# Kernel optimization log

Measured on AMD Instinct MI355X. Metric: run time of the kernel, lower is better.

Reference implementation:

```python
import jax, jax.numpy as jnp
import numpy as np

N_SRC = 50000
N_DST = 10000
E = 1600000
H = 1
F = 128
NEG_SLOPE = 0.2  # GAT default leaky_relu slope


def setup_inputs() -> dict:
    key = jax.random.key(0)
    k1, k2, k3, k4, k5, k6 = jax.random.split(key, 6)
    x_src = jax.random.normal(k1, (N_SRC, H, F), dtype=jnp.float32)
    x_dst = jax.random.normal(k2, (N_DST, H, F), dtype=jnp.float32)
    attn_l = jax.random.normal(k3, (1, H, F), dtype=jnp.float32)
    attn_r = jax.random.normal(k4, (1, H, F), dtype=jnp.float32)
    src_idx = jax.random.randint(k5, (E,), 0, N_SRC, dtype=jnp.int64 if jax.config.jax_enable_x64 else jnp.int32)
    dst_idx = jnp.sort(jax.random.randint(k6, (E,), 0, N_DST, dtype=jnp.int64 if jax.config.jax_enable_x64 else jnp.int32))
    return {"x_src": x_src, "x_dst": x_dst, "attn_l": attn_l, "attn_r": attn_r,
            "src_idx": src_idx, "dst_idx": dst_idx}


def reference(x_src, x_dst, attn_l, attn_r, src_idx, dst_idx):
    n_dst = x_dst.shape[0]
    # per-node attention logits: [N, H]
    el = (x_src * attn_l).sum(axis=-1)
    er = (x_dst * attn_r).sum(axis=-1)
    # per-edge score e = leaky_relu(el[u] + er[v]): [E, H]
    e = jax.nn.leaky_relu(el[src_idx] + er[dst_idx], negative_slope=NEG_SLOPE)
    ex = jnp.exp(e)
    # segment-sum over destination neighborhoods: [N_dst, H]
    sum_ex = jax.ops.segment_sum(ex, dst_idx, num_segments=n_dst)
    attention = ex / sum_ex[dst_idx]  # [E, H]
    # attention-weighted gather of src features, scattered to dst: [N_dst, H, F]
    msg = attention[..., None] * x_src[src_idx]
    out = jax.ops.segment_sum(msg, dst_idx, num_segments=n_dst)
    return out
```

## Files before the change

### kernel.cpp

```cpp
#include <hip/hip_runtime.h>
#include <hip/hip_fp16.h>

#define F 128
#define NEG_SLOPE 0.2f
#define NB 4

#define FMA_MIX_LO(acc, w, h) \
    asm("v_fma_mix_f32 %0, %1, %2, %0 op_sel:[0,0,0] op_sel_hi:[0,1,0]" \
        : "+v"(acc) : "v"(w), "v"(h))
#define FMA_MIX_HI(acc, w, h) \
    asm("v_fma_mix_f32 %0, %1, %2, %0 op_sel:[0,1,0] op_sel_hi:[0,1,0]" \
        : "+v"(acc) : "v"(w), "v"(h))

__global__ __launch_bounds__(256)
void prep_kernel(const float* __restrict__ x_src, const float* __restrict__ attn_l,
                 float* __restrict__ el, __half2* __restrict__ xh, int n_src,
                 const float* __restrict__ x_dst, const float* __restrict__ attn_r,
                 float* __restrict__ er, int n_dst,
                 const int* __restrict__ dst_idx, int* __restrict__ offs, int E,
                 int nlog) {
    if ((int)blockIdx.x < nlog) {
        int wave = blockIdx.x * 4 + (threadIdx.x >> 6);
        int lane = threadIdx.x & 63;
        int half = lane >> 5;
        int l32  = lane & 31;
        int row  = wave * 2 + half;
        const float* x; const float* attn; float* o; int r; bool is_src;
        if (row < n_src)              { x = x_src; attn = attn_l; o = el; r = row; is_src = true; }
        else if (row < n_src + n_dst) { x = x_dst; attn = attn_r; o = er; r = row - n_src; is_src = false; }
        else return;
        float4 xv = reinterpret_cast<const float4*>(x)[(size_t)r * 32 + l32];
        float4 av = reinterpret_cast<const float4*>(attn)[l32];
        if (xh && is_src) {
            __half2 h0 = __floats2half2_rn(xv.x, xv.y);
            __half2 h1 = __floats2half2_rn(xv.z, xv.w);
            uint2 u;
            u.x = *reinterpret_cast<unsigned int*>(&h0);
            u.y = *reinterpret_cast<unsigned int*>(&h1);
            reinterpret_cast<uint2*>(xh)[(size_t)r * 32 + l32] = u;
        }
        float s = xv.x * av.x + xv.y * av.y + xv.z * av.z + xv.w * av.w;
        #pragma unroll
        for (int o_ = 16; o_ > 0; o_ >>= 1) s += __shfl_xor(s, o_, 64);
        if (l32 == 0) o[r] = s;
    } else {
        int e = ((int)blockIdx.x - nlog) * 256 + threadIdx.x;
        if (e >= E) return;
        int d = dst_idx[e];
        int prev = (e == 0) ? -1 : dst_idx[e - 1];
        for (int v = prev + 1; v <= d; ++v) offs[v] = e;
        if (e == E - 1)
            for (int v = d + 1; v <= n_dst; ++v) offs[v] = E;
    }
}

__global__ __launch_bounds__(256)
void reorder_kernel(const int* __restrict__ src_idx, const int* __restrict__ offs,
                    const float* __restrict__ el, const float* __restrict__ er,
                    int2* __restrict__ ew, int* __restrict__ boffs,
                    int n_dst, float inv_bdiv) {
    int v = blockIdx.x * 4 + (threadIdx.x >> 6);
    if (v >= n_dst) return;
    int lane = threadIdx.x & 63;
    int start = offs[v], end = offs[v + 1];
    float erv = er[v];
    unsigned long long lt = (1ULL << lane) - 1ULL;

    int c0 = 0, c1 = 0, c2 = 0, c3 = 0;
    for (int base = start; base < end; base += 64) {
        int e = base + lane;
        int b = -1;
        if (e < end) {
            int s = src_idx[e];
            b = (int)((float)s * inv_bdiv);
            if (b > NB - 1) b = NB - 1;
        }
        c0 += __popcll(__ballot(b == 0));
        c1 += __popcll(__ballot(b == 1));
        c2 += __popcll(__ballot(b == 2));
        c3 += __popcll(__ballot(b == 3));
    }
    int base0 = start;
    int base1 = base0 + c0;
    int base2 = base1 + c1;
    int base3 = base2 + c2;
    if (lane == 0) {
        boffs[(size_t)v * (NB + 1) + 0] = base0;
        boffs[(size_t)v * (NB + 1) + 1] = base1;
        boffs[(size_t)v * (NB + 1) + 2] = base2;
        boffs[(size_t)v * (NB + 1) + 3] = base3;
        boffs[(size_t)v * (NB + 1) + 4] = base3 + c3;
    }

    for (int base = start; base < end; base += 64) {
        int e = base + lane;
        int b = -1, s = 0;
        float w = 0.f;
        if (e < end) {
            s = src_idx[e];
            b = (int)((float)s * inv_bdiv);
            if (b > NB - 1) b = NB - 1;
            float l = el[s] + erv;
            l = l > 0.f ? l : NEG_SLOPE * l;
            w = __expf(l);
        }
        int2 payload = make_int2(s * (F / 8), __float_as_int(w));
        unsigned long long m;
        m = __ballot(b == 0);
        if (b == 0) ew[base0 + __popcll(m & lt)] = payload;
        base0 += __popcll(m);
        m = __ballot(b == 1);
        if (b == 1) ew[base1 + __popcll(m & lt)] = payload;
        base1 += __popcll(m);
        m = __ballot(b == 2);
        if (b == 2) ew[base2 + __popcll(m & lt)] = payload;
        base2 += __popcll(m);
        m = __ballot(b == 3);
        if (b == 3) ew[base3 + __popcll(m & lt)] = payload;
        base3 += __popcll(m);
    }
}

__global__ __launch_bounds__(256)
void agg_slice_kernel(const __half2* __restrict__ xh,
                      const int2* __restrict__ ew,
                      const int* __restrict__ boffs,
                      float* __restrict__ part, float* __restrict__ pden,
                      int n_dst) {
    int b   = blockIdx.x & (NB - 1);
    int v   = ((int)blockIdx.x >> 2) * 16 + (threadIdx.x >> 4);
    if (v >= n_dst) return;
    int l16 = threadIdx.x & 15;

    int s0e = boffs[(size_t)v * (NB + 1) + b];
    int s1e = boffs[(size_t)v * (NB + 1) + b + 1];

    const float4* x4h = reinterpret_cast<const float4*>(xh);

    float a[8];
    #pragma unroll
    for (int k = 0; k < 8; ++k) a[k] = 0.f;
    float den = 0.f;

    int cnt  = s1e - s0e;
    int full = cnt & ~3;
    for (int it = 0; it < full; it += 4) {
        int2 q0 = ew[s0e + it];
        int2 q1 = ew[s0e + it + 1];
        int2 q2 = ew[s0e + it + 2];
        int2 q3 = ew[s0e + it + 3];
        float w0 = __int_as_float(q0.y);
        float w1 = __int_as_float(q1.y);
        float w2 = __int_as_float(q2.y);
        float w3 = __int_as_float(q3.y);
        float4 r0 = x4h[q0.x + l16];
        float4 r1 = x4h[q1.x + l16];
        float4 r2 = x4h[q2.x + l16];
        float4 r3 = x4h[q3.x + l16];
        den += w0 + w1 + w2 + w3;
        const unsigned int* u0 = reinterpret_cast<const unsigned int*>(&r0);
        const unsigned int* u1 = reinterpret_cast<const unsigned int*>(&r1);
        const unsigned int* u2 = reinterpret_cast<const unsigned int*>(&r2);
        const unsigned int* u3 = reinterpret_cast<const unsigned int*>(&r3);
        #pragma unroll
        for (int k = 0; k < 4; ++k) {
            FMA_MIX_LO(a[2*k],   w0, u0[k]);
            FMA_MIX_HI(a[2*k+1], w0, u0[k]);
            FMA_MIX_LO(a[2*k],   w1, u1[k]);
            FMA_MIX_HI(a[2*k+1], w1, u1[k]);
            FMA_MIX_LO(a[2*k],   w2, u2[k]);
            FMA_MIX_HI(a[2*k+1], w2, u2[k]);
            FMA_MIX_LO(a[2*k],   w3, u3[k]);
            FMA_MIX_HI(a[2*k+1], w3, u3[k]);
        }
    }
    for (int it = full; it < cnt; ++it) {
        int2 q = ew[s0e + it];
        float w = __int_as_float(q.y);
        den += w;
        float4 r = x4h[q.x + l16];
        const unsigned int* u = reinterpret_cast<const unsigned int*>(&r);
        #pragma unroll
        for (int k = 0; k < 4; ++k) {
            FMA_MIX_LO(a[2*k],   w, u[k]);
            FMA_MIX_HI(a[2*k+1], w, u[k]);
        }
    }

    float4* pp = reinterpret_cast<float4*>(&part[((size_t)b * n_dst + v) * F + l16 * 8]);
    pp[0] = make_float4(a[0], a[1], a[2], a[3]);
    pp[1] = make_float4(a[4], a[5], a[6], a[7]);
    if (l16 == 0) pden[(size_t)b * n_dst + v] = den;
}

__global__ __launch_bounds__(256)
void combine_kernel(const float* __restrict__ part, const float* __restrict__ pden,
                    float* __restrict__ out, int n_dst) {
    int t = blockIdx.x * 256 + threadIdx.x;
    int total = n_dst * (F / 4);
    if (t >= total) return;
    int v = t >> 5;
    const float4* p4 = reinterpret_cast<const float4*>(part);
    float4 n = make_float4(0.f, 0.f, 0.f, 0.f);
    float den = 0.f;
    #pragma unroll
    for (int b = 0; b < NB; ++b) {
        float4 u = p4[(size_t)b * total + t];
        n.x += u.x; n.y += u.y; n.z += u.z; n.w += u.w;
        den += pden[(size_t)b * n_dst + v];
    }
    float inv = (den > 0.f) ? 1.f / den : 0.f;
    reinterpret_cast<float4*>(out)[t] = make_float4(n.x*inv, n.y*inv, n.z*inv, n.w*inv);
}

template<bool H>
__global__ __launch_bounds__(256)
void agg_full_kernel(const __half2* __restrict__ xh, const float* __restrict__ x_src,
                     const float* __restrict__ el, const float* __restrict__ er,
                     const int* __restrict__ src_idx, const int* __restrict__ offs,
                     float* __restrict__ out, int n_dst) {
    int v = blockIdx.x * 4 + (threadIdx.x >> 6);
    if (v >= n_dst) return;
    int lane = threadIdx.x & 63;
    int g    = lane >> 4;
    int l16  = lane & 15;

    int start = offs[v];
    int end   = offs[v + 1];
    int count = end - start;
    float erv = er[v];

    const float4* x4h = reinterpret_cast<const float4*>(xh);
    const float4* x4f = reinterpret_cast<const float4*>(x_src);

    float a0[8];
    #pragma unroll
    for (int k = 0; k < 8; ++k) a0[k] = 0.f;
    float d0 = 0.f;

    for (int e = start + g; e < end; e += 4) {
        int s = src_idx[e];
        float l = el[s] + erv;
        l = l > 0.f ? l : NEG_SLOPE * l;
        float w = __expf(l);
        d0 += w;
        if (H) {
            float4 r = x4h[(size_t)s * (F / 8) + l16];
            const unsigned int* u = reinterpret_cast<const unsigned int*>(&r);
            #pragma unroll
            for (int k = 0; k < 4; ++k) {
                FMA_MIX_LO(a0[2*k],   w, u[k]);
                FMA_MIX_HI(a0[2*k+1], w, u[k]);
            }
        } else {
            float4 p = x4f[(size_t)s * (F/4) + l16*2];
            float4 q = x4f[(size_t)s * (F/4) + l16*2 + 1];
            a0[0]+=w*p.x; a0[1]+=w*p.y; a0[2]+=w*p.z; a0[3]+=w*p.w;
            a0[4]+=w*q.x; a0[5]+=w*q.y; a0[6]+=w*q.z; a0[7]+=w*q.w;
        }
    }
    #pragma unroll
    for (int k = 0; k < 8; ++k) {
        a0[k] += __shfl_xor(a0[k], 16, 64);
        a0[k] += __shfl_xor(a0[k], 32, 64);
    }
    d0 += __shfl_xor(d0, 16, 64);
    d0 += __shfl_xor(d0, 32, 64);

    if (g == 0) {
        float inv = (count > 0) ? 1.f / d0 : 0.f;
        float4* dst = reinterpret_cast<float4*>(&out[(size_t)v * F + l16 * 8]);
        dst[0] = make_float4(a0[0]*inv, a0[1]*inv, a0[2]*inv, a0[3]*inv);
        dst[1] = make_float4(a0[4]*inv, a0[5]*inv, a0[6]*inv, a0[7]*inv);
    }
}

extern "C" void kernel_launch(void* const* d_in, const int* in_sizes, int n_in,
                              void* d_out, int out_size, void* d_ws, size_t ws_size,
                              hipStream_t stream) {
    const float* x_src   = (const float*)d_in[0];
    const float* x_dst   = (const float*)d_in[1];
    const float* attn_l  = (const float*)d_in[2];
    const float* attn_r  = (const float*)d_in[3];
    const int*   src_idx = (const int*)d_in[4];
    const int*   dst_idx = (const int*)d_in[5];

    int n_src = in_sizes[0] / F;
    int n_dst = in_sizes[1] / F;
    int E     = in_sizes[4];

    float* out  = (float*)d_out;
    float* el   = (float*)d_ws;
    float* er   = el + n_src;
    int*   offs = (int*)(er + n_dst);
    uintptr_t p = (uintptr_t)(offs + n_dst + 1);
    p = (p + 15) & ~(uintptr_t)15;
    __half2* xh = (__half2*)p;
    uintptr_t q = p + (size_t)n_src * F * sizeof(__half);
    q = (q + 15) & ~(uintptr_t)15;
    int2*  ew    = (int2*)q;
    int*   boffs = (int*)(ew + E);
    uintptr_t r  = (uintptr_t)(boffs + (size_t)n_dst * (NB + 1));
    r = (r + 15) & ~(uintptr_t)15;
    float* part  = (float*)r;
    float* pden  = part + (size_t)NB * n_dst * F;

    size_t need_fp16 = (q - (uintptr_t)d_ws);
    size_t need_full = ((uintptr_t)(pden + (size_t)NB * n_dst)) - (uintptr_t)d_ws;
    bool fp16ok = ws_size >= need_fp16;
    bool fullok = ws_size >= need_full;

    int nlog = (n_src + n_dst + 7) / 8;
    int noff = (E + 255) / 256;
    prep_kernel<<<nlog + noff, 256, 0, stream>>>(
        x_src, attn_l, el, fp16ok ? xh : nullptr, n_src,
        x_dst, attn_r, er, n_dst, dst_idx, offs, E, nlog);

    if (fullok && fp16ok) {
        int bdiv = (n_src + NB - 1) / NB;
        float inv_bdiv = 1.0f / (float)bdiv;
        reorder_kernel<<<(n_dst + 3) / 4, 256, 0, stream>>>(
            src_idx, offs, el, er, ew, boffs, n_dst, inv_bdiv);
        int nblk = ((n_dst + 15) / 16) * NB;
        agg_slice_kernel<<<nblk, 256, 0, stream>>>(
            xh, ew, boffs, part, pden, n_dst);
        combine_kernel<<<(n_dst * (F / 4) + 255) / 256, 256, 0, stream>>>(
            part, pden, out, n_dst);
    } else if (fp16ok) {
        agg_full_kernel<true><<<(n_dst + 3) / 4, 256, 0, stream>>>(
            xh, nullptr, el, er, src_idx, offs, out, n_dst);
    } else {
        agg_full_kernel<false><<<(n_dst + 3) / 4, 256, 0, stream>>>(
            nullptr, x_src, el, er, src_idx, offs, out, n_dst);
    }
}
```

Baseline: 73.69 us.

## Move fp16 conversion into reorder kernel and batch edge loads with nontemporal hints

Moves the fp32-to-fp16 conversion of x_src out of the logits kernel and into extra blocks of the reorder kernel, so the conversion runs alongside the edge reordering instead of lengthening the first kernel. The aggregation loop now unrolls over 8 edges instead of 4 and reads edge records as 64-bit nontemporal loads. Partial results and edge records are written with nontemporal stores. The trade-off is higher register pressure from the wider unroll, and the nontemporal hints may hurt if the data is reused from cache.

New measurement: 89.56 us. 1.22x slower.

```diff
diff --git a/kernel.cpp b/kernel.cpp
--- a/kernel.cpp
+++ b/kernel.cpp
@@ -4,6 +4,7 @@
 #define F 128
 #define NEG_SLOPE 0.2f
 #define NB 4
+typedef unsigned long long ull;
 
 #define FMA_MIX_LO(acc, w, h) \
     asm("v_fma_mix_f32 %0, %1, %2, %0 op_sel:[0,0,0] op_sel_hi:[0,1,0]" \
@@ -13,32 +14,24 @@
         : "+v"(acc) : "v"(w), "v"(h))
 
 __global__ __launch_bounds__(256)
-void prep_kernel(const float* __restrict__ x_src, const float* __restrict__ attn_l,
-                 float* __restrict__ el, __half2* __restrict__ xh, int n_src,
-                 const float* __restrict__ x_dst, const float* __restrict__ attn_r,
-                 float* __restrict__ er, int n_dst,
-                 const int* __restrict__ dst_idx, int* __restrict__ offs, int E,
-                 int nlog) {
+void logits_offs_kernel(const float* __restrict__ x_src, const float* __restrict__ attn_l,
+                        float* __restrict__ el, int n_src,
+                        const float* __restrict__ x_dst, const float* __restrict__ attn_r,
+                        float* __restrict__ er, int n_dst,
+                        const int* __restrict__ dst_idx, int* __restrict__ offs, int E,
+                        int nlog) {
     if ((int)blockIdx.x < nlog) {
         int wave = blockIdx.x * 4 + (threadIdx.x >> 6);
         int lane = threadIdx.x & 63;
         int half = lane >> 5;
         int l32  = lane & 31;
         int row  = wave * 2 + half;
-        const float* x; const float* attn; float* o; int r; bool is_src;
-        if (row < n_src)              { x = x_src; attn = attn_l; o = el; r = row; is_src = true; }
-        else if (row < n_src + n_dst) { x = x_dst; attn = attn_r; o = er; r = row - n_src; is_src = false; }
+        const float* x; const float* attn; float* o; int r;
+        if (row < n_src)              { x = x_src; attn = attn_l; o = el; r = row; }
+        else if (row < n_src + n_dst) { x = x_dst; attn = attn_r; o = er; r = row - n_src; }
         else return;
         float4 xv = reinterpret_cast<const float4*>(x)[(size_t)r * 32 + l32];
         float4 av = reinterpret_cast<const float4*>(attn)[l32];
-        if (xh && is_src) {
-            __half2 h0 = __floats2half2_rn(xv.x, xv.y);
-            __half2 h1 = __floats2half2_rn(xv.z, xv.w);
-            uint2 u;
-            u.x = *reinterpret_cast<unsigned int*>(&h0);
-            u.y = *reinterpret_cast<unsigned int*>(&h1);
-            reinterpret_cast<uint2*>(xh)[(size_t)r * 32 + l32] = u;
-        }
         float s = xv.x * av.x + xv.y * av.y + xv.z * av.z + xv.w * av.w;
         #pragma unroll
         for (int o_ = 16; o_ > 0; o_ >>= 1) s += __shfl_xor(s, o_, 64);
@@ -55,69 +48,84 @@
 }
 
 __global__ __launch_bounds__(256)
-void reorder_kernel(const int* __restrict__ src_idx, const int* __restrict__ offs,
-                    const float* __restrict__ el, const float* __restrict__ er,
-                    int2* __restrict__ ew, int* __restrict__ boffs,
-                    int n_dst, float inv_bdiv) {
-    int v = blockIdx.x * 4 + (threadIdx.x >> 6);
-    if (v >= n_dst) return;
-    int lane = threadIdx.x & 63;
-    int start = offs[v], end = offs[v + 1];
-    float erv = er[v];
-    unsigned long long lt = (1ULL << lane) - 1ULL;
-
-    int c0 = 0, c1 = 0, c2 = 0, c3 = 0;
-    for (int base = start; base < end; base += 64) {
-        int e = base + lane;
-        int b = -1;
-        if (e < end) {
-            int s = src_idx[e];
-            b = (int)((float)s * inv_bdiv);
-            if (b > NB - 1) b = NB - 1;
-        }
-        c0 += __popcll(__ballot(b == 0));
-        c1 += __popcll(__ballot(b == 1));
-        c2 += __popcll(__ballot(b == 2));
-        c3 += __popcll(__ballot(b == 3));
-    }
-    int base0 = start;
-    int base1 = base0 + c0;
-    int base2 = base1 + c1;
-    int base3 = base2 + c2;
-    if (lane == 0) {
-        boffs[(size_t)v * (NB + 1) + 0] = base0;
-        boffs[(size_t)v * (NB + 1) + 1] = base1;
-        boffs[(size_t)v * (NB + 1) + 2] = base2;
-        boffs[(size_t)v * (NB + 1) + 3] = base3;
-        boffs[(size_t)v * (NB + 1) + 4] = base3 + c3;
-    }
-
-    for (int base = start; base < end; base += 64) {
-        int e = base + lane;
-        int b = -1, s = 0;
-        float w = 0.f;
-        if (e < end) {
-            s = src_idx[e];
-            b = (int)((float)s * inv_bdiv);
-            if (b > NB - 1) b = NB - 1;
-            float l = el[s] + erv;
-            l = l > 0.f ? l : NEG_SLOPE * l;
-            w = __expf(l);
-        }
-        int2 payload = make_int2(s * (F / 8), __float_as_int(w));
-        unsigned long long m;
-        m = __ballot(b == 0);
-        if (b == 0) ew[base0 + __popcll(m & lt)] = payload;
-        base0 += __popcll(m);
-        m = __ballot(b == 1);
-        if (b == 1) ew[base1 + __popcll(m & lt)] = payload;
-        base1 += __popcll(m);
-        m = __ballot(b == 2);
-        if (b == 2) ew[base2 + __popcll(m & lt)] = payload;
-        base2 += __popcll(m);
-        m = __ballot(b == 3);
-        if (b == 3) ew[base3 + __popcll(m & lt)] = payload;
-        base3 += __popcll(m);
+void reorder_convert_kernel(const int* __restrict__ src_idx, const int* __restrict__ offs,
+                            const float* __restrict__ el, const float* __restrict__ er,
+                            int2* __restrict__ ew, int* __restrict__ boffs,
+                            int n_dst, float inv_bdiv,
+                            const float* __restrict__ x_src, __half2* __restrict__ xh,
+                            int n_src, int nrb) {
+    if ((int)blockIdx.x < nrb) {
+        int v = blockIdx.x * 4 + (threadIdx.x >> 6);
+        if (v >= n_dst) return;
+        int lane = threadIdx.x & 63;
+        int start = offs[v], end = offs[v + 1];
+        float erv = er[v];
+        ull lt = (1ULL << lane) - 1ULL;
+
+        int c0 = 0, c1 = 0, c2 = 0, c3 = 0;
+        for (int base = start; base < end; base += 64) {
+            int e = base + lane;
+            int b = -1;
+            if (e < end) {
+                int s = src_idx[e];
+                b = (int)((float)s * inv_bdiv);
+                if (b > NB - 1) b = NB - 1;
+            }
+            c0 += __popcll(__ballot(b == 0));
+            c1 += __popcll(__ballot(b == 1));
+            c2 += __popcll(__ballot(b == 2));
+            c3 += __popcll(__ballot(b == 3));
+        }
+        int base0 = start;
+        int base1 = base0 + c0;
+        int base2 = base1 + c1;
+        int base3 = base2 + c2;
+        if (lane == 0) {
+            boffs[(size_t)v * (NB + 1) + 0] = base0;
+            boffs[(size_t)v * (NB + 1) + 1] = base1;
+            boffs[(size_t)v * (NB + 1) + 2] = base2;
+            boffs[(size_t)v * (NB + 1) + 3] = base3;
+            boffs[(size_t)v * (NB + 1) + 4] = base3 + c3;
+        }
+
+        for (int base = start; base < end; base += 64) {
+            int e = base + lane;
+            int b = -1, s = 0;
+            float w = 0.f;
+            if (e < end) {
+                s = src_idx[e];
+                b = (int)((float)s * inv_bdiv);
+                if (b > NB - 1) b = NB - 1;
+                float l = el[s] + erv;
+                l = l > 0.f ? l : NEG_SLOPE * l;
+                w = __expf(l);
+            }
+            ull pay = ((ull)__float_as_uint(w) << 32) | (unsigned)(s * (F / 8));
+            ull m;
+            m = __ballot(b == 0);
+            if (b == 0) __builtin_nontemporal_store(pay, (ull*)&ew[base0 + __popcll(m & lt)]);
+            base0 += __popcll(m);
+            m = __ballot(b == 1);
+            if (b == 1) __builtin_nontemporal_store(pay, (ull*)&ew[base1 + __popcll(m & lt)]);
+            base1 += __popcll(m);
+            m = __ballot(b == 2);
+            if (b == 2) __builtin_nontemporal_store(pay, (ull*)&ew[base2 + __popcll(m & lt)]);
+            base2 += __popcll(m);
+            m = __ballot(b == 3);
+            if (b == 3) __builtin_nontemporal_store(pay, (ull*)&ew[base3 + __popcll(m & lt)]);
+            base3 += __popcll(m);
+        }
+    } else {
+        int t = ((int)blockIdx.x - nrb) * 256 + threadIdx.x;
+        int total = n_src * (F / 4);
+        if (t >= total || xh == nullptr) return;
+        float4 xv = reinterpret_cast<const float4*>(x_src)[t];
+        __half2 h0 = __floats2half2_rn(xv.x, xv.y);
+        __half2 h1 = __floats2half2_rn(xv.z, xv.w);
+        uint2 u;
+        u.x = *reinterpret_cast<unsigned int*>(&h0);
+        u.y = *reinterpret_cast<unsigned int*>(&h1);
+        reinterpret_cast<uint2*>(xh)[t] = u;
     }
 }
 
@@ -136,6 +144,7 @@
     int s1e = boffs[(size_t)v * (NB + 1) + b + 1];
 
     const float4* x4h = reinterpret_cast<const float4*>(xh);
+    const ull*    ewu = reinterpret_cast<const ull*>(ew);
 
     float a[8];
     #pragma unroll
@@ -143,54 +152,50 @@
     float den = 0.f;
 
     int cnt  = s1e - s0e;
-    int full = cnt & ~3;
-    for (int it = 0; it < full; it += 4) {
-        int2 q0 = ew[s0e + it];
-        int2 q1 = ew[s0e + it + 1];
-        int2 q2 = ew[s0e + it + 2];
-        int2 q3 = ew[s0e + it + 3];
-        float w0 = __int_as_float(q0.y);
-        float w1 = __int_as_float(q1.y);
-        float w2 = __int_as_float(q2.y);
-        float w3 = __int_as_float(q3.y);
-        float4 r0 = x4h[q0.x + l16];
-        float4 r1 = x4h[q1.x + l16];
-        float4 r2 = x4h[q2.x + l16];
-        float4 r3 = x4h[q3.x + l16];
-        den += w0 + w1 + w2 + w3;
-        const unsigned int* u0 = reinterpret_cast<const unsigned int*>(&r0);
-        const unsigned int* u1 = reinterpret_cast<const unsigned int*>(&r1);
-        const unsigned int* u2 = reinterpret_cast<const unsigned int*>(&r2);
-        const unsigned int* u3 = reinterpret_cast<const unsigned int*>(&r3);
-        #pragma unroll
-        for (int k = 0; k < 4; ++k) {
-            FMA_MIX_LO(a[2*k],   w0, u0[k]);
-            FMA_MIX_HI(a[2*k+1], w0, u0[k]);
-            FMA_MIX_LO(a[2*k],   w1, u1[k]);
-            FMA_MIX_HI(a[2*k+1], w1, u1[k]);
-            FMA_MIX_LO(a[2*k],   w2, u2[k]);
-            FMA_MIX_HI(a[2*k+1], w2, u2[k]);
-            FMA_MIX_LO(a[2*k],   w3, u3[k]);
-            FMA_MIX_HI(a[2*k+1], w3, u3[k]);
+    int full = cnt & ~7;
+    for (int it = 0; it < full; it += 8) {
+        ull q[8];
+        #pragma unroll
+        for (int k = 0; k < 8; ++k) q[k] = __builtin_nontemporal_load(&ewu[s0e + it + k]);
+        float4 r[8];
+        #pragma unroll
+        for (int k = 0; k < 8; ++k) r[k] = x4h[(int)(unsigned)(q[k] & 0xffffffffu) + l16];
+        #pragma unroll
+        for (int k = 0; k < 8; ++k) {
+            float w = __uint_as_float((unsigned)(q[k] >> 32));
+            den += w;
+            const unsigned int* u = reinterpret_cast<const unsigned int*>(&r[k]);
+            #pragma unroll
+            for (int j = 0; j < 4; ++j) {
+                FMA_MIX_LO(a[2*j],   w, u[j]);
+                FMA_MIX_HI(a[2*j+1], w, u[j]);
+            }
         }
     }
     for (int it = full; it < cnt; ++it) {
-        int2 q = ew[s0e + it];
-        float w = __int_as_float(q.y);
+        ull q = __builtin_nontemporal_load(&ewu[s0e + it]);
+        float w = __uint_as_float((unsigned)(q >> 32));
         den += w;
-        float4 r = x4h[q.x + l16];
+        float4 r = x4h[(int)(unsigned)(q & 0xffffffffu) + l16];
         const unsigned int* u = reinterpret_cast<const unsigned int*>(&r);
         #pragma unroll
-        for (int k = 0; k < 4; ++k) {
-            FMA_MIX_LO(a[2*k],   w, u[k]);
-            FMA_MIX_HI(a[2*k+1], w, u[k]);
-        }
-    }
-
-    float4* pp = reinterpret_cast<float4*>(&part[((size_t)b * n_dst + v) * F + l16 * 8]);
-    pp[0] = make_float4(a[0], a[1], a[2], a[3]);
-    pp[1] = make_float4(a[4], a[5], a[6], a[7]);
-    if (l16 == 0) pden[(size_t)b * n_dst + v] = den;
+        for (int j = 0; j < 4; ++j) {
+            FMA_MIX_LO(a[2*j],   w, u[j]);
+            FMA_MIX_HI(a[2*j+1], w, u[j]);
+        }
+    }
+
+    ull* pp = reinterpret_cast<ull*>(&part[((size_t)b * n_dst + v) * F + l16 * 8]);
+    union { float f[2]; ull u; } w01, w23, w45, w67;
+    w01.f[0] = a[0]; w01.f[1] = a[1];
+    w23.f[0] = a[2]; w23.f[1] = a[3];
+    w45.f[0] = a[4]; w45.f[1] = a[5];
+    w67.f[0] = a[6]; w67.f[1] = a[7];
+    __builtin_nontemporal_store(w01.u, pp + 0);
+    __builtin_nontemporal_store(w23.u, pp + 1);
+    __builtin_nontemporal_store(w45.u, pp + 2);
+    __builtin_nontemporal_store(w67.u, pp + 3);
+    if (l16 == 0) __builtin_nontemporal_store(den, &pden[(size_t)b * n_dst + v]);
 }
 
 __global__ __launch_bounds__(256)
@@ -312,21 +317,24 @@
 
     int nlog = (n_src + n_dst + 7) / 8;
     int noff = (E + 255) / 256;
-    prep_kernel<<<nlog + noff, 256, 0, stream>>>(
-        x_src, attn_l, el, fp16ok ? xh : nullptr, n_src,
-        x_dst, attn_r, er, n_dst, dst_idx, offs, E, nlog);
+    logits_offs_kernel<<<nlog + noff, 256, 0, stream>>>(
+        x_src, attn_l, el, n_src, x_dst, attn_r, er, n_dst, dst_idx, offs, E, nlog);
+
+    int ncv = fp16ok ? (n_src * (F / 4) + 255) / 256 : 0;
 
     if (fullok && fp16ok) {
         int bdiv = (n_src + NB - 1) / NB;
         float inv_bdiv = 1.0f / (float)bdiv;
-        reorder_kernel<<<(n_dst + 3) / 4, 256, 0, stream>>>(
-            src_idx, offs, el, er, ew, boffs, n_dst, inv_bdiv);
+        int nrb = (n_dst + 3) / 4;
+        reorder_convert_kernel<<<nrb + ncv, 256, 0, stream>>>(
+            src_idx, offs, el, er, ew, boffs, n_dst, inv_bdiv, x_src, xh, n_src, nrb);
         int nblk = ((n_dst + 15) / 16) * NB;
-        agg_slice_kernel<<<nblk, 256, 0, stream>>>(
-            xh, ew, boffs, part, pden, n_dst);
+        agg_slice_kernel<<<nblk, 256, 0, stream>>>(xh, ew, boffs, part, pden, n_dst);
         combine_kernel<<<(n_dst * (F / 4) + 255) / 256, 256, 0, stream>>>(
             part, pden, out, n_dst);
     } else if (fp16ok) {
+        reorder_convert_kernel<<<ncv, 256, 0, stream>>>(
+            src_idx, offs, el, er, nullptr, nullptr, n_dst, 0.f, x_src, xh, n_src, 0);
         agg_full_kernel<true><<<(n_dst + 3) / 4, 256, 0, stream>>>(
             xh, nullptr, el, er, src_idx, offs, out, n_dst);
     } else {
```
